# Kernel tuning notes

Measured on AMD Instinct MI355X. Metric: run time of the kernel, lower is better.

## Reference

```python
import jax, jax.numpy as jnp
import numpy as np

NUM_CLASSES = 10000
NUM_PROXIES = 10
EMB_DIM = 128
MARGIN_DELTA = 0.01
LAMBDA_ = 20.0
GAMMA = 0.1


def setup_inputs() -> dict:
    key = jax.random.key(0)
    k1, k2, k3 = jax.random.split(key, 3)
    features = jax.random.normal(k1, (256, EMB_DIM), dtype=jnp.float32)
    labels = jax.random.randint(k2, (256,), 0, NUM_CLASSES, dtype=jnp.int64)
    # xavier_uniform over (num_classes, num_proxies, emb_dim): fan_in=emb_dim (last dim),
    # fan_out=num_proxies (torch treats dim0 as fan_out-ish for >2D; use standard gain=1)
    fan_in, fan_out = NUM_PROXIES * EMB_DIM, NUM_CLASSES  # torch: fan_in = prod(dims[1:]), fan_out = dims[0]
    limit = float(np.sqrt(6.0 / (fan_in + fan_out)))
    proxies = jax.random.uniform(k3, (NUM_CLASSES, NUM_PROXIES, EMB_DIM),
                                 dtype=jnp.float32, minval=-limit, maxval=limit)
    return {"features": features, "labels": labels, "proxies": proxies}


def reference(features, labels, proxies):
    B = features.shape[0]
    split = B // 2
    # dot_products: [B, C, K]
    dots = jnp.einsum('bd,ckd->bck', features, proxies)
    w = jax.nn.softmax(dots / GAMMA, axis=2)          # softmax over proxies
    S_ic = jnp.sum(w * dots, axis=2)                   # [B, C]
    S_avg = (S_ic[:split] + S_ic[split:]) * 0.5        # [split, C]
    lab = labels[:split]
    idx = jnp.arange(split)
    S_correct = S_avg[idx, lab] - MARGIN_DELTA         # [split]
    S_scaled = LAMBDA_ * S_avg
    S_correct_scaled = LAMBDA_ * S_correct
    S_corrected = S_scaled.at[idx, lab].set(S_correct_scaled)
    denom = jax.nn.logsumexp(S_corrected, axis=1)
    loss = -jnp.mean(S_correct_scaled - denom)
    return loss
```

## Files before the change

### kernel.cpp

```cpp
#include <hip/hip_runtime.h>
#include <hip/hip_bf16.h>

#define NUM_CLASSES 10000
#define NUM_PROXIES 10
#define EMB_DIM 128
#define HALF_B 128
#define MARGIN_DELTA 0.01f
#define LAMBDA_ 20.0f
#define INV_GAMMA 10.0f

#define CB 8
#define ROWS (CB * NUM_PROXIES)
#define MF 5
#define KSTEPS 4
#define NTILE 1250
#define TSTRIDE 164

#define SBYTES (ROWS * EMB_DIM * 2)
#define COFF   SBYTES
#define SMEMSZ (COFF + TSTRIDE * 256)

typedef __bf16 bf16x8 __attribute__((ext_vector_type(8)));
typedef __bf16 bf16x4 __attribute__((ext_vector_type(4)));
typedef float f32x4 __attribute__((ext_vector_type(4)));
typedef unsigned short ushort_t;

__device__ __forceinline__ unsigned int pk2bf(float a, float b) {
    __bf16 ha = (__bf16)a, hb = (__bf16)b;
    return (unsigned int)__builtin_bit_cast(ushort_t, ha) |
           ((unsigned int)__builtin_bit_cast(ushort_t, hb) << 16);
}
__device__ __forceinline__ float bf2f(unsigned int u16) {
    unsigned int x = u16 << 16;
    return __builtin_bit_cast(float, x);
}

__global__ __launch_bounds__(256, 2) void compute_S_kernel(
    const float* __restrict__ prox,
    const float* __restrict__ feat,
    const int* __restrict__ labels,
    float* __restrict__ Ps,
    float* __restrict__ sc)
{
    __shared__ __align__(16) char smem[SMEMSZ];

    const int tid     = threadIdx.x;
    const int lane    = tid & 63;
    const int w       = tid >> 6;
    const int l15     = lane & 15;
    const int g       = lane >> 4;
    const int tileIdx = blockIdx.x;
    const int lab     = labels[tid & 127];

    const char* pbase = (const char*)prox + (size_t)tileIdx * (ROWS * EMB_DIM * 4);
    float4 sv[10];
    #pragma unroll
    for (int j = 0; j < 10; ++j)
        sv[j] = *(const float4*)(pbase + ((size_t)(j * 256 + tid) << 4));

    bf16x8 bfrag[4][KSTEPS];
    #pragma unroll
    for (int nf = 0; nf < 4; ++nf) {
        #pragma unroll
        for (int t = 0; t < KSTEPS; ++t) {
            int col = w * 64 + nf * 16 + l15;
            const float4* fp = (const float4*)(feat + (size_t)col * EMB_DIM + t * 32 + g * 8);
            float4 v0 = fp[0], v1 = fp[1];
            bfrag[nf][t] = (bf16x8){ (__bf16)v0.x, (__bf16)v0.y, (__bf16)v0.z, (__bf16)v0.w,
                                     (__bf16)v1.x, (__bf16)v1.y, (__bf16)v1.z, (__bf16)v1.w };
        }
    }

    #pragma unroll
    for (int j = 0; j < 10; ++j) {
        int cid = j * 256 + tid;
        int row = cid >> 5;
        int c32 = cid & 31;
        int off = row * 256 + ((((c32 >> 1) ^ (row & 7))) << 4) + ((c32 & 1) << 3);
        bf16x4 o = { (__bf16)sv[j].x, (__bf16)sv[j].y, (__bf16)sv[j].z, (__bf16)sv[j].w };
        *(bf16x4*)(smem + off) = o;
    }

    __syncthreads();

    f32x4 acc[MF][4];
    #pragma unroll
    for (int mf = 0; mf < MF; ++mf)
        #pragma unroll
        for (int nf = 0; nf < 4; ++nf)
            acc[mf][nf] = (f32x4){0.f, 0.f, 0.f, 0.f};

    __builtin_amdgcn_s_setprio(1);
    #pragma unroll
    for (int t = 0; t < KSTEPS; ++t) {
        #pragma unroll
        for (int mf = 0; mf < MF; ++mf) {
            int row = mf * 16 + l15;
            int ck  = (t * 4 + g) ^ (row & 7);
            bf16x8 a = *(const bf16x8*)(smem + row * 256 + (ck << 4));
            #pragma unroll
            for (int nf = 0; nf < 4; ++nf)
                acc[mf][nf] = __builtin_amdgcn_mfma_f32_16x16x32_bf16(
                    a, bfrag[nf][t], acc[mf][nf], 0, 0, 0);
        }
    }
    __builtin_amdgcn_s_setprio(0);

    char* C = smem + COFF;
    #pragma unroll
    for (int mf = 0; mf < MF; ++mf) {
        #pragma unroll
        for (int nf = 0; nf < 4; ++nf) {
            int col  = w * 64 + nf * 16 + l15;
            int rowb = mf * 16 + g * 4;
            unsigned int lo = pk2bf(acc[mf][nf][0], acc[mf][nf][1]);
            unsigned int hi = pk2bf(acc[mf][nf][2], acc[mf][nf][3]);
            char* p = C + col * TSTRIDE + rowb * 2;
            *(unsigned int*)p       = lo;
            *(unsigned int*)(p + 4) = hi;
        }
    }
    __syncthreads();

    const int colh  = tid & 127;
    const int chalf = tid >> 7;
    float lsum = 0.f;
    #pragma unroll
    for (int cl4 = 0; cl4 < 4; ++cl4) {
        int cl = chalf * 4 + cl4;
        float Ssum = 0.f;
        #pragma unroll
        for (int h = 0; h < 2; ++h) {
            const char* base = C + (colh + h * 128) * TSTRIDE + cl * 20;
            float d[10];
            #pragma unroll
            for (int p5 = 0; p5 < 5; ++p5) {
                unsigned int pr = *(const unsigned int*)(base + p5 * 4);
                d[2 * p5]     = bf2f(pr & 0xFFFFu);
                d[2 * p5 + 1] = bf2f(pr >> 16);
            }
            float sw = 0.f, sd = 0.f;
            #pragma unroll
            for (int k = 0; k < NUM_PROXIES; ++k) {
                float e = __expf(d[k] * INV_GAMMA);
                sw += e;
                sd += e * d[k];
            }
            Ssum += sd / sw;
        }
        float Savg = 0.5f * Ssum;
        int c = tileIdx * CB + cl;
        float x = LAMBDA_ * Savg;
        if (c == lab) {
            x -= LAMBDA_ * MARGIN_DELTA;
            sc[colh] = x;
        }
        lsum += __expf(x);
    }

    *(float*)(C + tid * TSTRIDE + 160) = lsum;
    __syncthreads();
    if (tid < HALF_B) {
        float a = *(const float*)(C + tid * TSTRIDE + 160);
        float b = *(const float*)(C + (tid + 128) * TSTRIDE + 160);
        Ps[(size_t)tileIdx * HALF_B + tid] = a + b;
    }
}

__global__ __launch_bounds__(256) void psum_kernel(
    const float* __restrict__ Ps,
    float* __restrict__ Psum2)
{
    const int b0  = blockIdx.x * 25;
    const int tid = threadIdx.x;
    const int r   = tid >> 5;
    const int c   = tid & 31;

    float4 s = make_float4(0.f, 0.f, 0.f, 0.f);
    #pragma unroll
    for (int j = 0; j < 4; ++j) {
        int b = r + 8 * j;
        if (b < 25) {
            float4 v = *(const float4*)(Ps + (size_t)(b0 + b) * HALF_B + c * 4);
            s.x += v.x; s.y += v.y; s.z += v.z; s.w += v.w;
        }
    }

    __shared__ float red[8][HALF_B];
    *(float4*)&red[r][c * 4] = s;
    __syncthreads();
    if (tid < HALF_B) {
        float t = 0.f;
        #pragma unroll
        for (int rr = 0; rr < 8; ++rr) t += red[rr][tid];
        Psum2[blockIdx.x * HALF_B + tid] = t;
    }
}

__global__ __launch_bounds__(128) void finalize_kernel(
    const float* __restrict__ Psum2,
    const float* __restrict__ sc,
    float* __restrict__ out)
{
    const int i = threadIdx.x;
    float t = 0.f;
    #pragma unroll
    for (int b = 0; b < 50; ++b) t += Psum2[b * HALF_B + i];
    float part = sc[i] - __logf(t);

    __shared__ float buf[HALF_B];
    buf[i] = part;
    __syncthreads();
    #pragma unroll
    for (int off = 64; off >= 1; off >>= 1) {
        if (i < off) buf[i] += buf[i + off];
        __syncthreads();
    }
    if (i == 0) out[0] = -buf[0] / (float)HALF_B;
}

extern "C" void kernel_launch(void* const* d_in, const int* in_sizes, int n_in,
                              void* d_out, int out_size, void* d_ws, size_t ws_size,
                              hipStream_t stream) {
    const float* feat   = (const float*)d_in[0];
    const int*   labels = (const int*)d_in[1];
    const float* prox   = (const float*)d_in[2];
    float* out = (float*)d_out;

    float* Ps    = (float*)d_ws;
    float* sc    = (float*)((char*)d_ws + 640000);
    float* Psum2 = (float*)((char*)d_ws + 640000 + 512);

    compute_S_kernel<<<NTILE, 256, 0, stream>>>(prox, feat, labels, Ps, sc);
    psum_kernel<<<50, 256, 0, stream>>>(Ps, Psum2);
    finalize_kernel<<<1, 128, 0, stream>>>(Psum2, sc, out);
}
```

Measured before the change: 34.52 us.

## Alias LDS tiles to raise occupancy and fuse finalize into reduce via last-block counter

The staging buffer for proxy tiles and the transposed output tile now share one LDS region, separated by an extra barrier. This shrinks the per-block LDS footprint so the launch bound can request three blocks per SIMD set instead of two. The separate finalize kernel is folded into the partial-sum kernel: an atomic counter picks the last block, which does the final log-sum and mean. That removes one kernel launch but adds a memset call and thread fences.

```diff
diff --git a/kernel.cpp b/kernel.cpp
--- a/kernel.cpp
+++ b/kernel.cpp
@@ -17,8 +17,7 @@
 #define TSTRIDE 164
 
 #define SBYTES (ROWS * EMB_DIM * 2)
-#define COFF   SBYTES
-#define SMEMSZ (COFF + TSTRIDE * 256)
+#define SMEMSZ (TSTRIDE * 256)
 
 typedef __bf16 bf16x8 __attribute__((ext_vector_type(8)));
 typedef __bf16 bf16x4 __attribute__((ext_vector_type(4)));
@@ -35,7 +34,7 @@
     return __builtin_bit_cast(float, x);
 }
 
-__global__ __launch_bounds__(256, 2) void compute_S_kernel(
+__global__ __launch_bounds__(256, 3) void compute_S_kernel(
     const float* __restrict__ prox,
     const float* __restrict__ feat,
     const int* __restrict__ labels,
@@ -106,7 +105,9 @@
     }
     __builtin_amdgcn_s_setprio(0);
 
-    char* C = smem + COFF;
+    __syncthreads();
+
+    char* C = smem;
     #pragma unroll
     for (int mf = 0; mf < MF; ++mf) {
         #pragma unroll
@@ -167,9 +168,12 @@
     }
 }
 
-__global__ __launch_bounds__(256) void psum_kernel(
+__global__ __launch_bounds__(256) void reduce_kernel(
     const float* __restrict__ Ps,
-    float* __restrict__ Psum2)
+    const float* __restrict__ sc,
+    float* __restrict__ Psum2,
+    unsigned int* __restrict__ ctr,
+    float* __restrict__ out)
 {
     const int b0  = blockIdx.x * 25;
     const int tid = threadIdx.x;
@@ -195,28 +199,28 @@
         for (int rr = 0; rr < 8; ++rr) t += red[rr][tid];
         Psum2[blockIdx.x * HALF_B + tid] = t;
     }
-}
-
-__global__ __launch_bounds__(128) void finalize_kernel(
-    const float* __restrict__ Psum2,
-    const float* __restrict__ sc,
-    float* __restrict__ out)
-{
-    const int i = threadIdx.x;
-    float t = 0.f;
-    #pragma unroll
-    for (int b = 0; b < 50; ++b) t += Psum2[b * HALF_B + i];
-    float part = sc[i] - __logf(t);
+
+    __threadfence();
+    __shared__ unsigned int amLast;
+    if (tid == 0) amLast = (atomicAdd(ctr, 1u) == 49u) ? 1u : 0u;
+    __syncthreads();
+    if (!amLast) return;
+    __threadfence();
 
     __shared__ float buf[HALF_B];
-    buf[i] = part;
+    if (tid < HALF_B) {
+        float t = 0.f;
+        #pragma unroll
+        for (int b = 0; b < 50; ++b) t += Psum2[b * HALF_B + tid];
+        buf[tid] = sc[tid] - __logf(t);
+    }
     __syncthreads();
     #pragma unroll
     for (int off = 64; off >= 1; off >>= 1) {
-        if (i < off) buf[i] += buf[i + off];
+        if (tid < off) buf[tid] += buf[tid + off];
         __syncthreads();
     }
-    if (i == 0) out[0] = -buf[0] / (float)HALF_B;
+    if (tid == 0) out[0] = -buf[0] / (float)HALF_B;
 }
 
 extern "C" void kernel_launch(void* const* d_in, const int* in_sizes, int n_in,
@@ -230,8 +234,9 @@
     float* Ps    = (float*)d_ws;
     float* sc    = (float*)((char*)d_ws + 640000);
     float* Psum2 = (float*)((char*)d_ws + 640000 + 512);
-
+    unsigned int* ctr = (unsigned int*)((char*)d_ws + 666112);
+
+    hipMemsetAsync(ctr, 0, 4, stream);
     compute_S_kernel<<<NTILE, 256, 0, stream>>>(prox, feat, labels, Ps, sc);
-    psum_kernel<<<50, 256, 0, stream>>>(Ps, Psum2);
-    finalize_kernel<<<1, 128, 0, stream>>>(Psum2, sc, out);
-}
+    reduce_kernel<<<50, 256, 0, stream>>>(Ps, sc, Psum2, ctr, out);
+}
```

After: 41.60 us. 20.5% more time.

## Prepack features to bf16 fragments and alias LDS to raise occupancy

Applied to the files above, without the earlier changes.

Adds a small pre-kernel that converts features to bf16 once and stores them in MFMA fragment order in workspace. The main kernel then does one 16-byte load per fragment instead of two float4 loads plus conversions in every block. The epilogue buffer now reuses the proxy tile's LDS region, guarded by an extra barrier, which shrinks LDS per block, and launch bounds are raised from 2 to 3 blocks per CU. The cost is one extra kernel launch, one more barrier, and possible register pressure or spills under the tighter launch bound.

```diff
diff --git a/kernel.cpp b/kernel.cpp
--- a/kernel.cpp
+++ b/kernel.cpp
@@ -17,8 +17,7 @@
 #define TSTRIDE 164
 
 #define SBYTES (ROWS * EMB_DIM * 2)
-#define COFF   SBYTES
-#define SMEMSZ (COFF + TSTRIDE * 256)
+#define SMEMSZ (TSTRIDE * 256)
 
 typedef __bf16 bf16x8 __attribute__((ext_vector_type(8)));
 typedef __bf16 bf16x4 __attribute__((ext_vector_type(4)));
@@ -35,9 +34,31 @@
     return __builtin_bit_cast(float, x);
 }
 
-__global__ __launch_bounds__(256, 2) void compute_S_kernel(
+__global__ __launch_bounds__(256) void pack_feat_kernel(
+    const float* __restrict__ feat,
+    bf16x8* __restrict__ featPack)
+{
+    const int gid = blockIdx.x * 256 + threadIdx.x;
+    #pragma unroll
+    for (int half = 0; half < 2; ++half) {
+        int e    = gid + half * 2048;
+        int lane = e & 63;
+        int t    = (e >> 6) & 3;
+        int nf   = (e >> 8) & 3;
+        int w    = (e >> 10) & 3;
+        int l15  = lane & 15;
+        int g    = lane >> 4;
+        int col  = w * 64 + nf * 16 + l15;
+        const float4* fp = (const float4*)(feat + (size_t)col * EMB_DIM + t * 32 + g * 8);
+        float4 v0 = fp[0], v1 = fp[1];
+        featPack[e] = (bf16x8){ (__bf16)v0.x, (__bf16)v0.y, (__bf16)v0.z, (__bf16)v0.w,
+                                (__bf16)v1.x, (__bf16)v1.y, (__bf16)v1.z, (__bf16)v1.w };
+    }
+}
+
+__global__ __launch_bounds__(256, 3) void compute_S_kernel(
     const float* __restrict__ prox,
-    const float* __restrict__ feat,
+    const bf16x8* __restrict__ featPack,
     const int* __restrict__ labels,
     float* __restrict__ Ps,
     float* __restrict__ sc)
@@ -60,16 +81,10 @@
 
     bf16x8 bfrag[4][KSTEPS];
     #pragma unroll
-    for (int nf = 0; nf < 4; ++nf) {
-        #pragma unroll
-        for (int t = 0; t < KSTEPS; ++t) {
-            int col = w * 64 + nf * 16 + l15;
-            const float4* fp = (const float4*)(feat + (size_t)col * EMB_DIM + t * 32 + g * 8);
-            float4 v0 = fp[0], v1 = fp[1];
-            bfrag[nf][t] = (bf16x8){ (__bf16)v0.x, (__bf16)v0.y, (__bf16)v0.z, (__bf16)v0.w,
-                                     (__bf16)v1.x, (__bf16)v1.y, (__bf16)v1.z, (__bf16)v1.w };
-        }
-    }
+    for (int nf = 0; nf < 4; ++nf)
+        #pragma unroll
+        for (int t = 0; t < KSTEPS; ++t)
+            bfrag[nf][t] = featPack[((w * 4 + nf) * 4 + t) * 64 + lane];
 
     #pragma unroll
     for (int j = 0; j < 10; ++j) {
@@ -106,7 +121,9 @@
     }
     __builtin_amdgcn_s_setprio(0);
 
-    char* C = smem + COFF;
+    __syncthreads();
+
+    char* C = smem;
     #pragma unroll
     for (int mf = 0; mf < MF; ++mf) {
         #pragma unroll
@@ -230,8 +247,10 @@
     float* Ps    = (float*)d_ws;
     float* sc    = (float*)((char*)d_ws + 640000);
     float* Psum2 = (float*)((char*)d_ws + 640000 + 512);
-
-    compute_S_kernel<<<NTILE, 256, 0, stream>>>(prox, feat, labels, Ps, sc);
+    bf16x8* featPack = (bf16x8*)((char*)d_ws + 666112);
+
+    pack_feat_kernel<<<8, 256, 0, stream>>>(feat, featPack);
+    compute_S_kernel<<<NTILE, 256, 0, stream>>>(prox, featPack, labels, Ps, sc);
     psum_kernel<<<50, 256, 0, stream>>>(Ps, Psum2);
     finalize_kernel<<<1, 128, 0, stream>>>(Psum2, sc, out);
 }
```

After: 30.13 us. -12.7%, faster.
